# Performance work log

Hardware: AMD Instinct MI355X
Metric: run time of the kernel (lower is better)

## Reference

```python
import jax, jax.numpy as jnp
import numpy as np

B, F, H, E, O = 512, 512, 512, 8, 512  # batch, feature, hidden, experts, out_frame


def setup_inputs() -> dict:
    key = jax.random.key(0)
    ks = jax.random.split(key, 14)
    u = lambda k, shape, s: jax.random.uniform(k, shape, jnp.float32) * s
    return {
        "x": jax.random.normal(ks[0], (B, F), jnp.float32),
        # gating MLP params (torch Linear: y = x @ W.T + b)
        "gw0": u(ks[1], (H, F), 0.04) - 0.02,
        "gb0": jnp.zeros((H,), jnp.float32),
        "gw1": u(ks[2], (H, H), 0.04) - 0.02,
        "gb1": jnp.zeros((H,), jnp.float32),
        "gw2": u(ks[3], (E, H), 0.04) - 0.02,
        "gb2": jnp.zeros((E,), jnp.float32),
        # expert weight/bias banks
        "alpha0": u(ks[4], (E, H, F), 0.01),
        "beta0": jnp.zeros((E, H, 1), jnp.float32),
        "alpha1": u(ks[5], (E, H, H), 0.01),
        "beta1": jnp.zeros((E, H, 1), jnp.float32),
        "alpha2": u(ks[6], (E, O, H), 0.01),
        "beta2": jnp.zeros((E, O, 1), jnp.float32),
    }


def reference(x, gw0, gb0, gw1, gb1, gw2, gb2,
              alpha0, beta0, alpha1, beta1, alpha2, beta2):
    # gating network
    h = jax.nn.elu(x @ gw0.T + gb0)
    h = jax.nn.elu(h @ gw1.T + gb1)
    g = jax.nn.softmax(h @ gw2.T + gb2, axis=1)  # [B, E]

    # per-sample blended weights (sum over experts of gate-scaled expert mats)
    blend_w = lambda a: jnp.einsum('be,ehf->bhf', g, a)
    blend_b = lambda b: jnp.einsum('be,eh->bh', g, b[..., 0])

    # per-sample 3-layer MLP (bmm with vector rhs == batched matvec)
    H1 = jax.nn.elu(jnp.einsum('bhf,bf->bh', blend_w(alpha0), x) + blend_b(beta0))
    H2 = jax.nn.elu(jnp.einsum('bhf,bf->bh', blend_w(alpha1), H1) + blend_b(beta1))
    H3 = jnp.einsum('bof,bf->bo', blend_w(alpha2), H2) + blend_b(beta2)
    return H3
```

## Files before the change

kernel.cpp:

```cpp
#include <hip/hip_runtime.h>
#include <hip/hip_bf16.h>
#include <math.h>

enum { Bq = 512, Fq = 512, Hq = 512, Eq = 8, Oq = 512 };

typedef __attribute__((ext_vector_type(8))) short short8;
typedef __attribute__((ext_vector_type(4))) float floatx4;

static __device__ __forceinline__ unsigned short f2bf(float f) {
  unsigned u = __float_as_uint(f);
  u += 0x7fffu + ((u >> 16) & 1u);
  return (unsigned short)(u >> 16);
}
static __device__ __forceinline__ float bf2f(unsigned short h) {
  return __uint_as_float(((unsigned)h) << 16);
}
static __device__ __forceinline__ float elu1(float v) {
  return v > 0.f ? v : (__expf(v) - 1.f);
}

typedef __attribute__((address_space(1))) const unsigned int gu32;
typedef __attribute__((address_space(3))) unsigned int lu32;
static __device__ __forceinline__ void gld16(const unsigned short* g,
                                             unsigned short* l) {
  __builtin_amdgcn_global_load_lds((gu32*)g, (lu32*)l, 16, 0, 0);
}

static __device__ __forceinline__ int swz(int q, int r) {
  return (q & ~7) | ((q ^ r) & 7);
}

static __device__ __forceinline__ void cvt_chunk(const float* __restrict__ src,
                                                 unsigned short* __restrict__ dst,
                                                 int chunk, int tid) {
  int j = chunk * 256 + tid;
  float4 v = ((const float4*)src)[j];
  ushort4 o;
  o.x = f2bf(v.x); o.y = f2bf(v.y); o.z = f2bf(v.z); o.w = f2bf(v.w);
  *(ushort4*)(dst + 4 * (size_t)j) = o;
}

static __device__ __forceinline__ short8 cvt8(const float* __restrict__ p) {
  float4 v0 = *(const float4*)p, v1 = *(const float4*)(p + 4);
  short8 o;
  o[0] = (short)f2bf(v0.x); o[1] = (short)f2bf(v0.y);
  o[2] = (short)f2bf(v0.z); o[3] = (short)f2bf(v0.w);
  o[4] = (short)f2bf(v1.x); o[5] = (short)f2bf(v1.y);
  o[6] = (short)f2bf(v1.z); o[7] = (short)f2bf(v1.w);
  return o;
}

template <int F32A, int F32W>
__global__ __launch_bounds__(256) void gating_cvt(
    const unsigned short* __restrict__ A, const float* __restrict__ Af,
    const unsigned short* __restrict__ W, const float* __restrict__ Wf,
    const float* __restrict__ bias, unsigned short* __restrict__ C,
    const float* __restrict__ asrc, unsigned short* __restrict__ adst) {
  const int blk = blockIdx.x, tid = threadIdx.x;
  if (blk >= 256) {
    cvt_chunk(asrc, adst, blk - 256, tid);
    return;
  }
  __shared__ unsigned short As[32 * 512];
  __shared__ unsigned short Ws[32 * 512];
  const int wave = tid >> 6, lane = tid & 63;
  const int wm = wave >> 1, wn = wave & 1;
  const int lr = lane & 15, lk = lane >> 4;
  const int m0 = (blk >> 4) * 32, n0 = (blk & 15) * 32;
#pragma unroll
  for (int i = 0; i < 8; i++) {
    int c = tid + i * 256;
    int r = c >> 6, q = c & 63;
    if (F32A) {
      *(short8*)&As[(r * 64 + swz(q, r)) * 8] =
          cvt8(Af + (size_t)(m0 + r) * 512 + q * 8);
    } else {
      gld16(&A[(size_t)(m0 + r) * 512 + swz(q, r) * 8], &As[(c & ~63) * 8]);
    }
  }
#pragma unroll
  for (int i = 0; i < 8; i++) {
    int c = tid + i * 256;
    int r = c >> 6, q = c & 63;
    if (F32W) {
      *(short8*)&Ws[(r * 64 + swz(q, r)) * 8] =
          cvt8(Wf + (size_t)(n0 + r) * 512 + q * 8);
    } else {
      gld16(&W[(size_t)(n0 + r) * 512 + swz(q, r) * 8], &Ws[(c & ~63) * 8]);
    }
  }
  __syncthreads();
  const int rA = wm * 16 + lr, rB = wn * 16 + lr;
  floatx4 ac[4];
#pragma unroll
  for (int j = 0; j < 4; j++) ac[j] = (floatx4){0.f, 0.f, 0.f, 0.f};
#pragma unroll
  for (int t = 0; t < 4; t++) {
#pragma unroll
    for (int j = 0; j < 4; j++) {
      int q = ((j * 128 + t * 32) >> 3) + lk;
      short8 av = *(const short8*)&As[rA * 512 + swz(q, rA) * 8];
      short8 bv = *(const short8*)&Ws[rB * 512 + swz(q, rB) * 8];
      ac[j] = __builtin_amdgcn_mfma_f32_16x16x32_bf16(av, bv, ac[j], 0, 0, 0);
    }
  }
  floatx4 acc = (ac[0] + ac[1]) + (ac[2] + ac[3]);
  int n = n0 + wn * 16 + lr;
  float bn = bias[n];
#pragma unroll
  for (int r = 0; r < 4; r++) {
    int m = m0 + wm * 16 + lk * 4 + r;
    C[(size_t)m * 512 + n] = f2bf(elu1(acc[r] + bn));
  }
}

__global__ __launch_bounds__(256) void gate_fused(
    const unsigned short* __restrict__ G1,
    const float* __restrict__ gw2,
    const float* __restrict__ gb2,
    float* __restrict__ g,
    const float* __restrict__ asrc, unsigned short* __restrict__ adst,
    float* __restrict__ outz) {
  const int blk = blockIdx.x, tid = threadIdx.x;
  if (blk >= 384) {
    cvt_chunk(asrc, adst, blk - 384, tid);
    return;
  }
  if (blk >= 128) {
    ((float4*)outz)[(blk - 128) * 256 + tid] = (float4){0.f, 0.f, 0.f, 0.f};
    return;
  }
  const int wave = tid >> 6, lane = tid & 63;
  const int b = blk * 4 + wave;
  float xv[8];
#pragma unroll
  for (int t = 0; t < 8; t++) xv[t] = bf2f(G1[(size_t)b * Hq + t * 64 + lane]);
  float le[Eq];
#pragma unroll
  for (int e = 0; e < Eq; e++) {
    float p = 0.f;
#pragma unroll
    for (int t = 0; t < 8; t++)
      p += xv[t] * gw2[(size_t)e * Hq + t * 64 + lane];
#pragma unroll
    for (int o = 32; o > 0; o >>= 1) p += __shfl_xor(p, o);
    le[e] = p + gb2[e];
  }
  float m = le[0];
#pragma unroll
  for (int e = 1; e < Eq; e++) m = fmaxf(m, le[e]);
  float s = 0.f;
#pragma unroll
  for (int e = 0; e < Eq; e++) {
    le[e] = __expf(le[e] - m);
    s += le[e];
  }
  float inv = 1.f / s;
  if (lane == 0) {
#pragma unroll
    for (int e = 0; e < Eq; e++) g[(size_t)b * Eq + e] = le[e] * inv;
  }
}

template <int FROMX, int FROMP, int ATOMIC>
__global__ __launch_bounds__(256) void expert_gemm(
    const float* __restrict__ Xf,
    const float* __restrict__ Pin,
    const unsigned short* __restrict__ Wb,
    const float* __restrict__ g,
    const float* __restrict__ beta,
    float* __restrict__ Pout) {
  __shared__ unsigned short As[32 * 256];
  __shared__ unsigned short Ws[2][32 * 256];
  const int tid = threadIdx.x;
  const int wave = tid >> 6, lane = tid & 63;
  const int wm = wave >> 1, wn = wave & 1;
  const int lr = lane & 15, lk = lane >> 4;
  const int m0 = blockIdx.y * 32, n0 = blockIdx.x * 32;
  const int kz = blockIdx.z, kbeg = kz * 256;

  if (FROMP) {
#pragma unroll
    for (int i = 0; i < 4; i++) {
      int c = tid + i * 256;
      int r = c >> 5, q = c & 31;
      const float* p0 = Pin + (size_t)(m0 + r) * 512 + kbeg + q * 8;
      const float* p1 = p0 + (size_t)Bq * Hq;
      float4 x0 = *(const float4*)p0, x1 = *(const float4*)(p0 + 4);
      float4 y0 = *(const float4*)p1, y1 = *(const float4*)(p1 + 4);
      short8 o;
      o[0] = (short)f2bf(elu1(x0.x + y0.x));
      o[1] = (short)f2bf(elu1(x0.y + y0.y));
      o[2] = (short)f2bf(elu1(x0.z + y0.z));
      o[3] = (short)f2bf(elu1(x0.w + y0.w));
      o[4] = (short)f2bf(elu1(x1.x + y1.x));
      o[5] = (short)f2bf(elu1(x1.y + y1.y));
      o[6] = (short)f2bf(elu1(x1.z + y1.z));
      o[7] = (short)f2bf(elu1(x1.w + y1.w));
      *(short8*)&As[(r * 32 + swz(q, r)) * 8] = o;
    }
  } else if (FROMX) {
#pragma unroll
    for (int i = 0; i < 4; i++) {
      int c = tid + i * 256;
      int r = c >> 5, q = c & 31;
      *(short8*)&As[(r * 32 + swz(q, r)) * 8] =
          cvt8(Xf + (size_t)(m0 + r) * 512 + kbeg + q * 8);
    }
  }
  auto stageW = [&](int e, int b) {
    const unsigned short* Wp = Wb + ((size_t)e * 512 + n0) * 512 + kbeg;
#pragma unroll
    for (int i = 0; i < 4; i++) {
      int c = tid + i * 256;
      int r = c >> 5, ql = c & 31;
      gld16(&Wp[(size_t)r * 512 + swz(ql, r) * 8], &Ws[b][(c & ~63) * 8]);
    }
  };
  stageW(0, 0);
  float g8[4][8];
#pragma unroll
  for (int r = 0; r < 4; r++) {
    int m = m0 + wm * 16 + lk * 4 + r;
    float4 ga = *(const float4*)&g[(size_t)m * 8];
    float4 gb = *(const float4*)&g[(size_t)m * 8 + 4];
    g8[r][0] = ga.x; g8[r][1] = ga.y; g8[r][2] = ga.z; g8[r][3] = ga.w;
    g8[r][4] = gb.x; g8[r][5] = gb.y; g8[r][6] = gb.z; g8[r][7] = gb.w;
  }

  const int rA = wm * 16 + lr, rB = wn * 16 + lr;
  short8 af[8];
  floatx4 fin = {0.f, 0.f, 0.f, 0.f};
#pragma unroll
  for (int e = 0; e < 8; e++) {
    __syncthreads();
    if (e < 7) stageW(e + 1, (e + 1) & 1);
    if (e == 0) {
#pragma unroll
      for (int s = 0; s < 8; s++)
        af[s] = *(const short8*)&As[rA * 256 + swz(s * 4 + lk, rA) * 8];
    }
    const unsigned short* wb = Ws[e & 1];
    floatx4 c0 = {0.f, 0.f, 0.f, 0.f}, c1 = {0.f, 0.f, 0.f, 0.f};
#pragma unroll
    for (int s = 0; s < 8; s++) {
      short8 bv = *(const short8*)&wb[rB * 256 + swz(s * 4 + lk, rB) * 8];
      if (s & 1)
        c1 = __builtin_amdgcn_mfma_f32_16x16x32_bf16(af[s], bv, c1, 0, 0, 0);
      else
        c0 = __builtin_amdgcn_mfma_f32_16x16x32_bf16(af[s], bv, c0, 0, 0, 0);
    }
    floatx4 ae = c0 + c1;
#pragma unroll
    for (int r = 0; r < 4; r++) fin[r] += g8[r][e] * ae[r];
  }

  int n = n0 + wn * 16 + lr;
  if (kz == 0) {
    float bv[8];
#pragma unroll
    for (int e = 0; e < 8; e++) bv[e] = beta[e * 512 + n];
#pragma unroll
    for (int r = 0; r < 4; r++) {
      float bs = 0.f;
#pragma unroll
      for (int e = 0; e < 8; e++) bs += g8[r][e] * bv[e];
      fin[r] += bs;
    }
  }
  if (ATOMIC) {
#pragma unroll
    for (int r = 0; r < 4; r++) {
      int m = m0 + wm * 16 + lk * 4 + r;
      atomicAdd(&Pout[(size_t)m * 512 + n], fin[r]);
    }
  } else {
    float* Po = Pout + (size_t)kz * Bq * Hq;
#pragma unroll
    for (int r = 0; r < 4; r++) {
      int m = m0 + wm * 16 + lk * 4 + r;
      Po[(size_t)m * 512 + n] = fin[r];
    }
  }
}

extern "C" void kernel_launch(void* const* d_in, const int* in_sizes, int n_in,
                              void* d_out, int out_size, void* d_ws,
                              size_t ws_size, hipStream_t stream) {
  const float* x = (const float*)d_in[0];
  const float* gw0 = (const float*)d_in[1];
  const float* gb0 = (const float*)d_in[2];
  const float* gw1 = (const float*)d_in[3];
  const float* gb1 = (const float*)d_in[4];
  const float* gw2 = (const float*)d_in[5];
  const float* gb2 = (const float*)d_in[6];
  const float* alpha0 = (const float*)d_in[7];
  const float* beta0 = (const float*)d_in[8];
  const float* alpha1 = (const float*)d_in[9];
  const float* beta1 = (const float*)d_in[10];
  const float* alpha2 = (const float*)d_in[11];
  const float* beta2 = (const float*)d_in[12];
  float* out = (float*)d_out;

  char* ws = (char*)d_ws;
  auto alloc = [&](size_t bytes) {
    char* p = ws;
    ws += (bytes + 255) & ~(size_t)255;
    return p;
  };
  unsigned short* a0b = (unsigned short*)alloc((size_t)Eq * Hq * Fq * 2);
  unsigned short* a1b = (unsigned short*)alloc((size_t)Eq * Hq * Hq * 2);
  unsigned short* a2b = (unsigned short*)alloc((size_t)Eq * Oq * Hq * 2);
  unsigned short* G0b = (unsigned short*)alloc((size_t)Bq * Hq * 2);
  unsigned short* G1b = (unsigned short*)alloc((size_t)Bq * Hq * 2);
  float* gates = (float*)alloc((size_t)Bq * Eq * 4);
  float* P1 = (float*)alloc((size_t)2 * Bq * Hq * 4);
  float* P2 = (float*)alloc((size_t)2 * Bq * Hq * 4);

  gating_cvt<1, 1><<<2304, 256, 0, stream>>>(nullptr, x, nullptr, gw0, gb0,
                                             G0b, alpha0, a0b);
  gating_cvt<0, 1><<<2304, 256, 0, stream>>>(G0b, nullptr, nullptr, gw1, gb1,
                                             G1b, alpha1, a1b);
  gate_fused<<<2432, 256, 0, stream>>>(G1b, gw2, gb2, gates, alpha2, a2b, out);

  dim3 ge(16, 16, 2);
  expert_gemm<1, 0, 0><<<ge, 256, 0, stream>>>(x, nullptr, a0b, gates, beta0,
                                               P1);
  expert_gemm<0, 1, 0><<<ge, 256, 0, stream>>>(nullptr, P1, a1b, gates, beta1,
                                               P2);
  expert_gemm<0, 1, 1><<<ge, 256, 0, stream>>>(nullptr, P2, a2b, gates, beta2,
                                               out);
}
```

Measured before the change: 134.5 us.

## Fuse all six launches into one persistent kernel with grid barriers

Replaces the six separate kernel launches (two gating GEMMs with conversion, gate softmax, three expert GEMMs) with a single 512-block persistent kernel. Phases are separated by software grid barriers built on atomic counters, which are zeroed with a memset before launch. The gating tile now stages K in two halves to fit a shared 48KB LDS buffer, and each extra block converts several weight chunks instead of one. This removes launch overhead and inter-kernel gaps but relies on all 512 blocks being co-resident, and uses fewer blocks for the weight conversion work.

Result: slower. 305.1 us (+126.8%).

```diff
diff --git a/kernel.cpp b/kernel.cpp
--- a/kernel.cpp
+++ b/kernel.cpp
@@ -2,7 +2,7 @@
 #include <hip/hip_bf16.h>
 #include <math.h>
 
-enum { Bq = 512, Fq = 512, Hq = 512, Eq = 8, Oq = 512 };
+enum { Bq = 512, Fq = 512, Hq = 512, Eq = 8, Oq = 512, NBLK = 512 };
 
 typedef __attribute__((ext_vector_type(8))) short short8;
 typedef __attribute__((ext_vector_type(4))) float floatx4;
@@ -50,58 +50,69 @@
   return o;
 }
 
-template <int F32A, int F32W>
-__global__ __launch_bounds__(256) void gating_cvt(
-    const unsigned short* __restrict__ A, const float* __restrict__ Af,
-    const unsigned short* __restrict__ W, const float* __restrict__ Wf,
-    const float* __restrict__ bias, unsigned short* __restrict__ C,
-    const float* __restrict__ asrc, unsigned short* __restrict__ adst) {
-  const int blk = blockIdx.x, tid = threadIdx.x;
-  if (blk >= 256) {
-    cvt_chunk(asrc, adst, blk - 256, tid);
-    return;
-  }
-  __shared__ unsigned short As[32 * 512];
-  __shared__ unsigned short Ws[32 * 512];
+static __device__ __forceinline__ void gsync(unsigned* bar) {
+  __syncthreads();
+  if (threadIdx.x == 0) {
+    __hip_atomic_fetch_add(bar, 1u, __ATOMIC_RELEASE,
+                           __HIP_MEMORY_SCOPE_AGENT);
+    unsigned tries = 0;
+    while (__hip_atomic_load(bar, __ATOMIC_RELAXED,
+                             __HIP_MEMORY_SCOPE_AGENT) < (unsigned)NBLK) {
+      __builtin_amdgcn_s_sleep(4);
+      if (++tries > (1u << 22)) break;
+    }
+    __builtin_amdgcn_fence(__ATOMIC_ACQUIRE, "agent");
+  }
+  __syncthreads();
+}
+
+template <int F32A>
+static __device__ void gating_tile(int blk, int tid, unsigned short* As,
+                                   unsigned short* Ws,
+                                   const unsigned short* __restrict__ A,
+                                   const float* __restrict__ Af,
+                                   const float* __restrict__ Wf,
+                                   const float* __restrict__ bias,
+                                   unsigned short* __restrict__ C) {
   const int wave = tid >> 6, lane = tid & 63;
   const int wm = wave >> 1, wn = wave & 1;
   const int lr = lane & 15, lk = lane >> 4;
   const int m0 = (blk >> 4) * 32, n0 = (blk & 15) * 32;
-#pragma unroll
-  for (int i = 0; i < 8; i++) {
-    int c = tid + i * 256;
-    int r = c >> 6, q = c & 63;
-    if (F32A) {
-      *(short8*)&As[(r * 64 + swz(q, r)) * 8] =
-          cvt8(Af + (size_t)(m0 + r) * 512 + q * 8);
-    } else {
-      gld16(&A[(size_t)(m0 + r) * 512 + swz(q, r) * 8], &As[(c & ~63) * 8]);
-    }
-  }
-#pragma unroll
-  for (int i = 0; i < 8; i++) {
-    int c = tid + i * 256;
-    int r = c >> 6, q = c & 63;
-    if (F32W) {
-      *(short8*)&Ws[(r * 64 + swz(q, r)) * 8] =
-          cvt8(Wf + (size_t)(n0 + r) * 512 + q * 8);
-    } else {
-      gld16(&W[(size_t)(n0 + r) * 512 + swz(q, r) * 8], &Ws[(c & ~63) * 8]);
-    }
-  }
-  __syncthreads();
   const int rA = wm * 16 + lr, rB = wn * 16 + lr;
   floatx4 ac[4];
 #pragma unroll
   for (int j = 0; j < 4; j++) ac[j] = (floatx4){0.f, 0.f, 0.f, 0.f};
 #pragma unroll
-  for (int t = 0; t < 4; t++) {
-#pragma unroll
-    for (int j = 0; j < 4; j++) {
-      int q = ((j * 128 + t * 32) >> 3) + lk;
-      short8 av = *(const short8*)&As[rA * 512 + swz(q, rA) * 8];
-      short8 bv = *(const short8*)&Ws[rB * 512 + swz(q, rB) * 8];
-      ac[j] = __builtin_amdgcn_mfma_f32_16x16x32_bf16(av, bv, ac[j], 0, 0, 0);
+  for (int kk = 0; kk < 2; kk++) {
+    const int kb = kk * 256;
+    if (kk) __syncthreads();
+#pragma unroll
+    for (int i = 0; i < 4; i++) {
+      int c = tid + i * 256;
+      int r = c >> 5, q = c & 31;
+      if (F32A) {
+        *(short8*)&As[(r * 32 + swz(q, r)) * 8] =
+            cvt8(Af + (size_t)(m0 + r) * 512 + kb + q * 8);
+      } else {
+        gld16(&A[(size_t)(m0 + r) * 512 + kb + swz(q, r) * 8],
+              &As[(c & ~63) * 8]);
+      }
+    }
+#pragma unroll
+    for (int i = 0; i < 4; i++) {
+      int c = tid + i * 256;
+      int r = c >> 5, q = c & 31;
+      *(short8*)&Ws[(r * 32 + swz(q, r)) * 8] =
+          cvt8(Wf + (size_t)(n0 + r) * 512 + kb + q * 8);
+    }
+    __syncthreads();
+#pragma unroll
+    for (int s = 0; s < 8; s++) {
+      int q = s * 4 + lk;
+      short8 av = *(const short8*)&As[rA * 256 + swz(q, rA) * 8];
+      short8 bv = *(const short8*)&Ws[rB * 256 + swz(q, rB) * 8];
+      ac[s & 3] =
+          __builtin_amdgcn_mfma_f32_16x16x32_bf16(av, bv, ac[s & 3], 0, 0, 0);
     }
   }
   floatx4 acc = (ac[0] + ac[1]) + (ac[2] + ac[3]);
@@ -114,22 +125,11 @@
   }
 }
 
-__global__ __launch_bounds__(256) void gate_fused(
-    const unsigned short* __restrict__ G1,
-    const float* __restrict__ gw2,
-    const float* __restrict__ gb2,
-    float* __restrict__ g,
-    const float* __restrict__ asrc, unsigned short* __restrict__ adst,
-    float* __restrict__ outz) {
-  const int blk = blockIdx.x, tid = threadIdx.x;
-  if (blk >= 384) {
-    cvt_chunk(asrc, adst, blk - 384, tid);
-    return;
-  }
-  if (blk >= 128) {
-    ((float4*)outz)[(blk - 128) * 256 + tid] = (float4){0.f, 0.f, 0.f, 0.f};
-    return;
-  }
+static __device__ void gate_softmax(int blk, int tid,
+                                    const unsigned short* __restrict__ G1,
+                                    const float* __restrict__ gw2,
+                                    const float* __restrict__ gb2,
+                                    float* __restrict__ g) {
   const int wave = tid >> 6, lane = tid & 63;
   const int b = blk * 4 + wave;
   float xv[8];
@@ -163,21 +163,21 @@
 }
 
 template <int FROMX, int FROMP, int ATOMIC>
-__global__ __launch_bounds__(256) void expert_gemm(
-    const float* __restrict__ Xf,
-    const float* __restrict__ Pin,
-    const unsigned short* __restrict__ Wb,
-    const float* __restrict__ g,
-    const float* __restrict__ beta,
-    float* __restrict__ Pout) {
-  __shared__ unsigned short As[32 * 256];
-  __shared__ unsigned short Ws[2][32 * 256];
-  const int tid = threadIdx.x;
+static __device__ void expert_phase(int blk, int tid, unsigned short* sm,
+                                    const float* __restrict__ Xf,
+                                    const float* __restrict__ Pin,
+                                    const unsigned short* __restrict__ Wb,
+                                    const float* __restrict__ g,
+                                    const float* __restrict__ beta,
+                                    float* __restrict__ Pout) {
+  unsigned short* As = sm;
+  unsigned short* const Wsb[2] = {sm + 8192, sm + 16384};
   const int wave = tid >> 6, lane = tid & 63;
   const int wm = wave >> 1, wn = wave & 1;
   const int lr = lane & 15, lk = lane >> 4;
-  const int m0 = blockIdx.y * 32, n0 = blockIdx.x * 32;
-  const int kz = blockIdx.z, kbeg = kz * 256;
+  const int n0 = (blk & 15) * 32;
+  const int m0 = ((blk >> 4) & 15) * 32;
+  const int kz = blk >> 8, kbeg = kz * 256;
 
   if (FROMP) {
 #pragma unroll
@@ -210,11 +210,12 @@
   }
   auto stageW = [&](int e, int b) {
     const unsigned short* Wp = Wb + ((size_t)e * 512 + n0) * 512 + kbeg;
+    unsigned short* W = Wsb[b];
 #pragma unroll
     for (int i = 0; i < 4; i++) {
       int c = tid + i * 256;
       int r = c >> 5, ql = c & 31;
-      gld16(&Wp[(size_t)r * 512 + swz(ql, r) * 8], &Ws[b][(c & ~63) * 8]);
+      gld16(&Wp[(size_t)r * 512 + swz(ql, r) * 8], &W[(c & ~63) * 8]);
     }
   };
   stageW(0, 0);
@@ -240,7 +241,7 @@
       for (int s = 0; s < 8; s++)
         af[s] = *(const short8*)&As[rA * 256 + swz(s * 4 + lk, rA) * 8];
     }
-    const unsigned short* wb = Ws[e & 1];
+    const unsigned short* wb = Wsb[e & 1];
     floatx4 c0 = {0.f, 0.f, 0.f, 0.f}, c1 = {0.f, 0.f, 0.f, 0.f};
 #pragma unroll
     for (int s = 0; s < 8; s++) {
@@ -282,6 +283,57 @@
       Po[(size_t)m * 512 + n] = fin[r];
     }
   }
+}
+
+__global__ __launch_bounds__(256, 2) void fused_moe(
+    const float* __restrict__ x, const float* __restrict__ gw0,
+    const float* __restrict__ gb0, const float* __restrict__ gw1,
+    const float* __restrict__ gb1, const float* __restrict__ gw2,
+    const float* __restrict__ gb2, const float* __restrict__ alpha0,
+    const float* __restrict__ beta0, const float* __restrict__ alpha1,
+    const float* __restrict__ beta1, const float* __restrict__ alpha2,
+    const float* __restrict__ beta2, unsigned short* __restrict__ a0b,
+    unsigned short* __restrict__ a1b, unsigned short* __restrict__ a2b,
+    unsigned short* __restrict__ G0b, unsigned short* __restrict__ G1b,
+    float* __restrict__ gates, float* __restrict__ P1, float* __restrict__ P2,
+    float* __restrict__ out, unsigned* __restrict__ bars) {
+  __shared__ unsigned short sm[24 * 1024];
+  const int blk = blockIdx.x, tid = threadIdx.x;
+
+  if (blk < 256) {
+    gating_tile<1>(blk, tid, sm, sm + 8192, nullptr, x, gw0, gb0, G0b);
+  } else {
+#pragma unroll
+    for (int i = 0; i < 8; i++)
+      cvt_chunk(alpha0, a0b, (blk - 256) * 8 + i, tid);
+  }
+  gsync(bars + 0);
+
+  if (blk < 256) {
+    gating_tile<0>(blk, tid, sm, sm + 8192, G0b, nullptr, gw1, gb1, G1b);
+  } else {
+#pragma unroll
+    for (int i = 0; i < 8; i++)
+      cvt_chunk(alpha1, a1b, (blk - 256) * 8 + i, tid);
+  }
+  gsync(bars + 16);
+
+  if (blk < 128) {
+    gate_softmax(blk, tid, G1b, gw2, gb2, gates);
+  } else if (blk < 384) {
+    ((float4*)out)[(blk - 128) * 256 + tid] = (float4){0.f, 0.f, 0.f, 0.f};
+  } else {
+#pragma unroll
+    for (int i = 0; i < 16; i++)
+      cvt_chunk(alpha2, a2b, (blk - 384) * 16 + i, tid);
+  }
+  gsync(bars + 32);
+
+  expert_phase<1, 0, 0>(blk, tid, sm, x, nullptr, a0b, gates, beta0, P1);
+  gsync(bars + 48);
+  expert_phase<0, 1, 0>(blk, tid, sm, nullptr, P1, a1b, gates, beta1, P2);
+  gsync(bars + 64);
+  expert_phase<0, 1, 1>(blk, tid, sm, nullptr, P2, a2b, gates, beta2, out);
 }
 
 extern "C" void kernel_launch(void* const* d_in, const int* in_sizes, int n_in,
@@ -316,18 +368,12 @@
   float* gates = (float*)alloc((size_t)Bq * Eq * 4);
   float* P1 = (float*)alloc((size_t)2 * Bq * Hq * 4);
   float* P2 = (float*)alloc((size_t)2 * Bq * Hq * 4);
-
-  gating_cvt<1, 1><<<2304, 256, 0, stream>>>(nullptr, x, nullptr, gw0, gb0,
-                                             G0b, alpha0, a0b);
-  gating_cvt<0, 1><<<2304, 256, 0, stream>>>(G0b, nullptr, nullptr, gw1, gb1,
-                                             G1b, alpha1, a1b);
-  gate_fused<<<2432, 256, 0, stream>>>(G1b, gw2, gb2, gates, alpha2, a2b, out);
-
-  dim3 ge(16, 16, 2);
-  expert_gemm<1, 0, 0><<<ge, 256, 0, stream>>>(x, nullptr, a0b, gates, beta0,
-                                               P1);
-  expert_gemm<0, 1, 0><<<ge, 256, 0, stream>>>(nullptr, P1, a1b, gates, beta1,
-                                               P2);
-  expert_gemm<0, 1, 1><<<ge, 256, 0, stream>>>(nullptr, P2, a2b, gates, beta2,
-                                               out);
-}
+  unsigned* bars = (unsigned*)alloc(512);
+
+  hipMemsetAsync(bars, 0, 512, stream);
+
+  fused_moe<<<512, 256, 0, stream>>>(x, gw0, gb0, gw1, gb1, gw2, gb2, alpha0,
+                                     beta0, alpha1, beta1, alpha2, beta2, a0b,
+                                     a1b, a2b, G0b, G1b, gates, P1, P2, out,
+                                     bars);
+}
```

## Fuse gating MLP into one kernel and deepen expert split-K to four

Applied to the files above, without the earlier changes.

Replaces the three gating launches with a single kernel in which each 32-row block computes both hidden gating layers and the softmax entirely on-chip, holding H1 in shared memory and folding the gw2 projection into the second layer's epilogue. The remaining blocks of that launch handle all three expert weight conversions and zeroing the output. The expert GEMMs now split K into four slices instead of two, giving more blocks, and the next layer sums four partial buffers. The cost is that the gating runs on only 16 blocks with serial loops over 16 column tiles, and there is more partial-sum traffic.

Result: slower. 184.7 us (+37.3%).

```diff
diff --git a/kernel.cpp b/kernel.cpp
--- a/kernel.cpp
+++ b/kernel.cpp
@@ -3,6 +3,7 @@
 #include <math.h>
 
 enum { Bq = 512, Fq = 512, Hq = 512, Eq = 8, Oq = 512 };
+enum { KZN = 4, KB = 512 / KZN };
 
 typedef __attribute__((ext_vector_type(8))) short short8;
 typedef __attribute__((ext_vector_type(4))) float floatx4;
@@ -50,171 +51,227 @@
   return o;
 }
 
-template <int F32A, int F32W>
-__global__ __launch_bounds__(256) void gating_cvt(
-    const unsigned short* __restrict__ A, const float* __restrict__ Af,
-    const unsigned short* __restrict__ W, const float* __restrict__ Wf,
-    const float* __restrict__ bias, unsigned short* __restrict__ C,
-    const float* __restrict__ asrc, unsigned short* __restrict__ adst) {
+__global__ __launch_bounds__(256, 2) void gate_all(
+    const float* __restrict__ x, const float* __restrict__ gw0,
+    const float* __restrict__ gb0, const float* __restrict__ gw1,
+    const float* __restrict__ gb1, const float* __restrict__ gw2,
+    const float* __restrict__ gb2,
+    const float* __restrict__ alpha0, unsigned short* __restrict__ a0b,
+    const float* __restrict__ alpha1, unsigned short* __restrict__ a1b,
+    const float* __restrict__ alpha2, unsigned short* __restrict__ a2b,
+    float* __restrict__ gates, float* __restrict__ outz) {
+  __shared__ unsigned short sm[32768];
   const int blk = blockIdx.x, tid = threadIdx.x;
-  if (blk >= 256) {
-    cvt_chunk(asrc, adst, blk - 256, tid);
+  if (blk >= 16) {
+    const int u0 = (blk - 16) * 8;
+    if (u0 < 2048) {
+#pragma unroll
+      for (int i = 0; i < 8; i++) cvt_chunk(alpha0, a0b, u0 + i, tid);
+    } else if (u0 < 4096) {
+#pragma unroll
+      for (int i = 0; i < 8; i++) cvt_chunk(alpha1, a1b, u0 - 2048 + i, tid);
+    } else if (u0 < 6144) {
+#pragma unroll
+      for (int i = 0; i < 8; i++) cvt_chunk(alpha2, a2b, u0 - 4096 + i, tid);
+    } else {
+#pragma unroll
+      for (int i = 0; i < 8; i++)
+        ((float4*)outz)[(size_t)(u0 - 6144 + i) * 256 + tid] =
+            (float4){0.f, 0.f, 0.f, 0.f};
+    }
     return;
   }
-  __shared__ unsigned short As[32 * 512];
-  __shared__ unsigned short Ws[32 * 512];
+  unsigned short* Ws0 = sm;
+  unsigned short* Ws1 = sm + 8192;
+  unsigned short* H1s = sm + 16384;
   const int wave = tid >> 6, lane = tid & 63;
   const int wm = wave >> 1, wn = wave & 1;
   const int lr = lane & 15, lk = lane >> 4;
-  const int m0 = (blk >> 4) * 32, n0 = (blk & 15) * 32;
-#pragma unroll
-  for (int i = 0; i < 8; i++) {
-    int c = tid + i * 256;
-    int r = c >> 6, q = c & 63;
-    if (F32A) {
-      *(short8*)&As[(r * 64 + swz(q, r)) * 8] =
-          cvt8(Af + (size_t)(m0 + r) * 512 + q * 8);
-    } else {
-      gld16(&A[(size_t)(m0 + r) * 512 + swz(q, r) * 8], &As[(c & ~63) * 8]);
-    }
-  }
-#pragma unroll
-  for (int i = 0; i < 8; i++) {
-    int c = tid + i * 256;
-    int r = c >> 6, q = c & 63;
-    if (F32W) {
-      *(short8*)&Ws[(r * 64 + swz(q, r)) * 8] =
-          cvt8(Wf + (size_t)(n0 + r) * 512 + q * 8);
-    } else {
-      gld16(&W[(size_t)(n0 + r) * 512 + swz(q, r) * 8], &Ws[(c & ~63) * 8]);
-    }
+  const int m0 = blk * 32;
+  const int rA = wm * 16 + lr, rB = wn * 16 + lr;
+
+  auto stage_w = [&](const float* __restrict__ gw, int nt, int kk,
+                     unsigned short* W) {
+#pragma unroll
+    for (int i = 0; i < 4; i++) {
+      int c = tid + i * 256;
+      int r = c >> 5, q = c & 31;
+      *(short8*)&W[(r * 32 + swz(q, r)) * 8] =
+          cvt8(gw + (size_t)(nt * 32 + r) * 512 + kk * 256 + q * 8);
+    }
+  };
+
+  short8 af[16];
+#pragma unroll
+  for (int i = 0; i < 16; i++)
+    af[i] = cvt8(x + (size_t)(m0 + rA) * 512 + (i * 4 + lk) * 8);
+  stage_w(gw0, 0, 0, Ws0);
+
+  float p[4][8];
+#pragma unroll
+  for (int r = 0; r < 4; r++)
+#pragma unroll
+    for (int e = 0; e < 8; e++) p[r][e] = 0.f;
+
+  for (int nt = 0; nt < 16; ++nt) {
+    floatx4 ac[4];
+#pragma unroll
+    for (int j = 0; j < 4; j++) ac[j] = (floatx4){0.f, 0.f, 0.f, 0.f};
+    __syncthreads();
+    stage_w(gw0, nt, 1, Ws1);
+#pragma unroll
+    for (int s = 0; s < 8; s++) {
+      short8 bv = *(const short8*)&Ws0[(rB * 32 + swz(s * 4 + lk, rB)) * 8];
+      ac[s & 3] =
+          __builtin_amdgcn_mfma_f32_16x16x32_bf16(af[s], bv, ac[s & 3], 0, 0, 0);
+    }
+    __syncthreads();
+    if (nt < 15) stage_w(gw0, nt + 1, 0, Ws0);
+#pragma unroll
+    for (int s = 0; s < 8; s++) {
+      short8 bv = *(const short8*)&Ws1[(rB * 32 + swz(s * 4 + lk, rB)) * 8];
+      ac[s & 3] = __builtin_amdgcn_mfma_f32_16x16x32_bf16(af[8 + s], bv,
+                                                          ac[s & 3], 0, 0, 0);
+    }
+    floatx4 acc = (ac[0] + ac[1]) + (ac[2] + ac[3]);
+    int col = nt * 32 + wn * 16 + lr;
+    float b0 = gb0[col];
+#pragma unroll
+    for (int r = 0; r < 4; r++) {
+      int ml = wm * 16 + lk * 4 + r;
+      H1s[(ml * 64 + swz(col >> 3, ml)) * 8 + (col & 7)] =
+          f2bf(elu1(acc[r] + b0));
+    }
+  }
+
+  stage_w(gw1, 0, 0, Ws0);
+
+  for (int nt = 0; nt < 16; ++nt) {
+    floatx4 ac[4];
+#pragma unroll
+    for (int j = 0; j < 4; j++) ac[j] = (floatx4){0.f, 0.f, 0.f, 0.f};
+    __syncthreads();
+    if (nt == 0) {
+#pragma unroll
+      for (int i = 0; i < 16; i++)
+        af[i] = *(const short8*)&H1s[(rA * 64 + swz(i * 4 + lk, rA)) * 8];
+    }
+    stage_w(gw1, nt, 1, Ws1);
+#pragma unroll
+    for (int s = 0; s < 8; s++) {
+      short8 bv = *(const short8*)&Ws0[(rB * 32 + swz(s * 4 + lk, rB)) * 8];
+      ac[s & 3] =
+          __builtin_amdgcn_mfma_f32_16x16x32_bf16(af[s], bv, ac[s & 3], 0, 0, 0);
+    }
+    __syncthreads();
+    if (nt < 15) stage_w(gw1, nt + 1, 0, Ws0);
+#pragma unroll
+    for (int s = 0; s < 8; s++) {
+      short8 bv = *(const short8*)&Ws1[(rB * 32 + swz(s * 4 + lk, rB)) * 8];
+      ac[s & 3] = __builtin_amdgcn_mfma_f32_16x16x32_bf16(af[8 + s], bv,
+                                                          ac[s & 3], 0, 0, 0);
+    }
+    floatx4 acc = (ac[0] + ac[1]) + (ac[2] + ac[3]);
+    int col = nt * 32 + wn * 16 + lr;
+    float b1 = gb1[col];
+    float vv[4];
+#pragma unroll
+    for (int r = 0; r < 4; r++) vv[r] = elu1(acc[r] + b1);
+#pragma unroll
+    for (int e = 0; e < 8; e++) {
+      float ge = gw2[(size_t)e * 512 + col];
+#pragma unroll
+      for (int r = 0; r < 4; r++) p[r][e] += vv[r] * ge;
+    }
+  }
+
+#pragma unroll
+  for (int off = 1; off <= 8; off <<= 1)
+#pragma unroll
+    for (int r = 0; r < 4; r++)
+#pragma unroll
+      for (int e = 0; e < 8; e++) p[r][e] += __shfl_xor(p[r][e], off);
+  float* scr = (float*)sm;
+  if (lr == 0) {
+#pragma unroll
+    for (int r = 0; r < 4; r++)
+#pragma unroll
+      for (int e = 0; e < 8; e++)
+        scr[(wm * 16 + lk * 4 + r) * 16 + wn * 8 + e] = p[r][e];
   }
   __syncthreads();
-  const int rA = wm * 16 + lr, rB = wn * 16 + lr;
-  floatx4 ac[4];
-#pragma unroll
-  for (int j = 0; j < 4; j++) ac[j] = (floatx4){0.f, 0.f, 0.f, 0.f};
-#pragma unroll
-  for (int t = 0; t < 4; t++) {
-#pragma unroll
-    for (int j = 0; j < 4; j++) {
-      int q = ((j * 128 + t * 32) >> 3) + lk;
-      short8 av = *(const short8*)&As[rA * 512 + swz(q, rA) * 8];
-      short8 bv = *(const short8*)&Ws[rB * 512 + swz(q, rB) * 8];
-      ac[j] = __builtin_amdgcn_mfma_f32_16x16x32_bf16(av, bv, ac[j], 0, 0, 0);
-    }
-  }
-  floatx4 acc = (ac[0] + ac[1]) + (ac[2] + ac[3]);
-  int n = n0 + wn * 16 + lr;
-  float bn = bias[n];
-#pragma unroll
-  for (int r = 0; r < 4; r++) {
-    int m = m0 + wm * 16 + lk * 4 + r;
-    C[(size_t)m * 512 + n] = f2bf(elu1(acc[r] + bn));
-  }
-}
-
-__global__ __launch_bounds__(256) void gate_fused(
-    const unsigned short* __restrict__ G1,
-    const float* __restrict__ gw2,
-    const float* __restrict__ gb2,
-    float* __restrict__ g,
-    const float* __restrict__ asrc, unsigned short* __restrict__ adst,
-    float* __restrict__ outz) {
-  const int blk = blockIdx.x, tid = threadIdx.x;
-  if (blk >= 384) {
-    cvt_chunk(asrc, adst, blk - 384, tid);
-    return;
-  }
-  if (blk >= 128) {
-    ((float4*)outz)[(blk - 128) * 256 + tid] = (float4){0.f, 0.f, 0.f, 0.f};
-    return;
-  }
-  const int wave = tid >> 6, lane = tid & 63;
-  const int b = blk * 4 + wave;
-  float xv[8];
-#pragma unroll
-  for (int t = 0; t < 8; t++) xv[t] = bf2f(G1[(size_t)b * Hq + t * 64 + lane]);
-  float le[Eq];
-#pragma unroll
-  for (int e = 0; e < Eq; e++) {
-    float p = 0.f;
-#pragma unroll
-    for (int t = 0; t < 8; t++)
-      p += xv[t] * gw2[(size_t)e * Hq + t * 64 + lane];
-#pragma unroll
-    for (int o = 32; o > 0; o >>= 1) p += __shfl_xor(p, o);
-    le[e] = p + gb2[e];
-  }
-  float m = le[0];
-#pragma unroll
-  for (int e = 1; e < Eq; e++) m = fmaxf(m, le[e]);
-  float s = 0.f;
-#pragma unroll
-  for (int e = 0; e < Eq; e++) {
-    le[e] = __expf(le[e] - m);
-    s += le[e];
-  }
-  float inv = 1.f / s;
-  if (lane == 0) {
-#pragma unroll
-    for (int e = 0; e < Eq; e++) g[(size_t)b * Eq + e] = le[e] * inv;
+  if (tid < 32) {
+    int row = tid;
+    float le[8], mx = -1e30f, ssum = 0.f;
+#pragma unroll
+    for (int e = 0; e < 8; e++) {
+      le[e] = scr[row * 16 + e] + scr[row * 16 + 8 + e] + gb2[e];
+      mx = fmaxf(mx, le[e]);
+    }
+#pragma unroll
+    for (int e = 0; e < 8; e++) {
+      le[e] = __expf(le[e] - mx);
+      ssum += le[e];
+    }
+    float inv = 1.f / ssum;
+#pragma unroll
+    for (int e = 0; e < 8; e++)
+      gates[(size_t)(m0 + row) * 8 + e] = le[e] * inv;
   }
 }
 
 template <int FROMX, int FROMP, int ATOMIC>
-__global__ __launch_bounds__(256) void expert_gemm(
+__global__ __launch_bounds__(256, 4) void expert_gemm(
     const float* __restrict__ Xf,
     const float* __restrict__ Pin,
     const unsigned short* __restrict__ Wb,
     const float* __restrict__ g,
     const float* __restrict__ beta,
     float* __restrict__ Pout) {
-  __shared__ unsigned short As[32 * 256];
-  __shared__ unsigned short Ws[2][32 * 256];
+  __shared__ unsigned short As[32 * KB];
+  __shared__ unsigned short Wsb[2][32 * KB];
   const int tid = threadIdx.x;
   const int wave = tid >> 6, lane = tid & 63;
   const int wm = wave >> 1, wn = wave & 1;
   const int lr = lane & 15, lk = lane >> 4;
   const int m0 = blockIdx.y * 32, n0 = blockIdx.x * 32;
-  const int kz = blockIdx.z, kbeg = kz * 256;
+  const int kz = blockIdx.z, kbeg = kz * KB;
 
   if (FROMP) {
 #pragma unroll
-    for (int i = 0; i < 4; i++) {
+    for (int i = 0; i < 2; i++) {
       int c = tid + i * 256;
-      int r = c >> 5, q = c & 31;
-      const float* p0 = Pin + (size_t)(m0 + r) * 512 + kbeg + q * 8;
-      const float* p1 = p0 + (size_t)Bq * Hq;
-      float4 x0 = *(const float4*)p0, x1 = *(const float4*)(p0 + 4);
-      float4 y0 = *(const float4*)p1, y1 = *(const float4*)(p1 + 4);
+      int r = c >> 4, q = c & 15;
+      const float* pp = Pin + (size_t)(m0 + r) * 512 + kbeg + q * 8;
+      float s[8] = {0.f, 0.f, 0.f, 0.f, 0.f, 0.f, 0.f, 0.f};
+#pragma unroll
+      for (int k = 0; k < KZN; k++) {
+        const float* pk = pp + (size_t)k * (Bq * Hq);
+        float4 va = *(const float4*)pk, vb = *(const float4*)(pk + 4);
+        s[0] += va.x; s[1] += va.y; s[2] += va.z; s[3] += va.w;
+        s[4] += vb.x; s[5] += vb.y; s[6] += vb.z; s[7] += vb.w;
+      }
       short8 o;
-      o[0] = (short)f2bf(elu1(x0.x + y0.x));
-      o[1] = (short)f2bf(elu1(x0.y + y0.y));
-      o[2] = (short)f2bf(elu1(x0.z + y0.z));
-      o[3] = (short)f2bf(elu1(x0.w + y0.w));
-      o[4] = (short)f2bf(elu1(x1.x + y1.x));
-      o[5] = (short)f2bf(elu1(x1.y + y1.y));
-      o[6] = (short)f2bf(elu1(x1.z + y1.z));
-      o[7] = (short)f2bf(elu1(x1.w + y1.w));
-      *(short8*)&As[(r * 32 + swz(q, r)) * 8] = o;
+#pragma unroll
+      for (int j = 0; j < 8; j++) o[j] = (short)f2bf(elu1(s[j]));
+      *(short8*)&As[(r * 16 + swz(q, r)) * 8] = o;
     }
   } else if (FROMX) {
 #pragma unroll
-    for (int i = 0; i < 4; i++) {
+    for (int i = 0; i < 2; i++) {
       int c = tid + i * 256;
-      int r = c >> 5, q = c & 31;
-      *(short8*)&As[(r * 32 + swz(q, r)) * 8] =
+      int r = c >> 4, q = c & 15;
+      *(short8*)&As[(r * 16 + swz(q, r)) * 8] =
           cvt8(Xf + (size_t)(m0 + r) * 512 + kbeg + q * 8);
     }
   }
   auto stageW = [&](int e, int b) {
     const unsigned short* Wp = Wb + ((size_t)e * 512 + n0) * 512 + kbeg;
 #pragma unroll
-    for (int i = 0; i < 4; i++) {
+    for (int i = 0; i < 2; i++) {
       int c = tid + i * 256;
-      int r = c >> 5, ql = c & 31;
-      gld16(&Wp[(size_t)r * 512 + swz(ql, r) * 8], &Ws[b][(c & ~63) * 8]);
+      int r = c >> 4, ql = c & 15;
+      gld16(&Wp[(size_t)r * 512 + swz(ql, r) * 8], &Wsb[b][(c & ~63) * 8]);
     }
   };
   stageW(0, 0);
@@ -229,7 +286,7 @@
   }
 
   const int rA = wm * 16 + lr, rB = wn * 16 + lr;
-  short8 af[8];
+  short8 af[4];
   floatx4 fin = {0.f, 0.f, 0.f, 0.f};
 #pragma unroll
   for (int e = 0; e < 8; e++) {
@@ -237,14 +294,14 @@
     if (e < 7) stageW(e + 1, (e + 1) & 1);
     if (e == 0) {
 #pragma unroll
-      for (int s = 0; s < 8; s++)
-        af[s] = *(const short8*)&As[rA * 256 + swz(s * 4 + lk, rA) * 8];
-    }
-    const unsigned short* wb = Ws[e & 1];
+      for (int s = 0; s < 4; s++)
+        af[s] = *(const short8*)&As[(rA * 16 + swz(s * 4 + lk, rA)) * 8];
+    }
+    const unsigned short* wb = Wsb[e & 1];
     floatx4 c0 = {0.f, 0.f, 0.f, 0.f}, c1 = {0.f, 0.f, 0.f, 0.f};
 #pragma unroll
-    for (int s = 0; s < 8; s++) {
-      short8 bv = *(const short8*)&wb[rB * 256 + swz(s * 4 + lk, rB) * 8];
+    for (int s = 0; s < 4; s++) {
+      short8 bv = *(const short8*)&wb[(rB * 16 + swz(s * 4 + lk, rB)) * 8];
       if (s & 1)
         c1 = __builtin_amdgcn_mfma_f32_16x16x32_bf16(af[s], bv, c1, 0, 0, 0);
       else
@@ -311,19 +368,13 @@
   unsigned short* a0b = (unsigned short*)alloc((size_t)Eq * Hq * Fq * 2);
   unsigned short* a1b = (unsigned short*)alloc((size_t)Eq * Hq * Hq * 2);
   unsigned short* a2b = (unsigned short*)alloc((size_t)Eq * Oq * Hq * 2);
-  unsigned short* G0b = (unsigned short*)alloc((size_t)Bq * Hq * 2);
-  unsigned short* G1b = (unsigned short*)alloc((size_t)Bq * Hq * 2);
   float* gates = (float*)alloc((size_t)Bq * Eq * 4);
-  float* P1 = (float*)alloc((size_t)2 * Bq * Hq * 4);
-  float* P2 = (float*)alloc((size_t)2 * Bq * Hq * 4);
-
-  gating_cvt<1, 1><<<2304, 256, 0, stream>>>(nullptr, x, nullptr, gw0, gb0,
-                                             G0b, alpha0, a0b);
-  gating_cvt<0, 1><<<2304, 256, 0, stream>>>(G0b, nullptr, nullptr, gw1, gb1,
-                                             G1b, alpha1, a1b);
-  gate_fused<<<2432, 256, 0, stream>>>(G1b, gw2, gb2, gates, alpha2, a2b, out);
-
-  dim3 ge(16, 16, 2);
+  float* P1 = (float*)alloc((size_t)KZN * Bq * Hq * 4);
+  float* P2 = (float*)alloc((size_t)KZN * Bq * Hq * 4);
+
+  gate_all<<<816, 256, 0, stream>>>(x, gw0, gb0, gw1, gb1, gw2, gb2, alpha0,
+                                    a0b, alpha1, a1b, alpha2, a2b, gates, out);
+  dim3 ge(16, 16, KZN);
   expert_gemm<1, 0, 0><<<ge, 256, 0, stream>>>(x, nullptr, a0b, gates, beta0,
                                                P1);
   expert_gemm<0, 1, 0><<<ge, 256, 0, stream>>>(nullptr, P1, a1b, gates, beta1,
```
